# Performance work log

Hardware: AMD Instinct MI355X
Metric: run time of the kernel (lower is better)

## Reference

```python
import jax, jax.numpy as jnp
import numpy as np

MASK_VAL = -1e9

def setup_inputs() -> dict:
    key = jax.random.key(0)
    kq, kk, kv, km = jax.random.split(key, 4)
    bz, lq, lk, d = 16, 2048, 2048, 64
    q = jax.random.normal(kq, (bz, lq, d), dtype=jnp.float32)
    k = jax.random.normal(kk, (bz, lk, d), dtype=jnp.float32)
    v = jax.random.normal(kv, (bz, lk, d), dtype=jnp.float32)
    # pad mask: True = masked-out position
    pad_mask = jax.random.randint(km, (bz, lq, lk), 0, 2) == 1
    return {"q": q, "k": k, "v": v, "pad_mask": pad_mask}

def reference(q, k, v, pad_mask):
    # scores: [bz, lq, lk]
    d = k.shape[-1]
    scores = jnp.einsum('bqd,bkd->bqk', q, k) / jnp.sqrt(jnp.asarray(d, q.dtype))
    scores = jnp.where(pad_mask, jnp.asarray(MASK_VAL, scores.dtype), scores)
    attn = jax.nn.softmax(scores, axis=-1)  # dropout inactive in eval mode
    out = jnp.einsum('bqk,bkd->bqd', attn, v)
    return out
```

## Files before the change

### kernel.cpp

```cpp
#include <hip/hip_runtime.h>
#include <hip/hip_bf16.h>
#include <cstdint>
#include <cstddef>

typedef __attribute__((ext_vector_type(8))) short  short8;
typedef __attribute__((ext_vector_type(4))) short  short4v;
typedef __attribute__((ext_vector_type(4))) float  f32x4;

#define BZ   16
#define LQ   2048
#define LK   2048
#define DD   64
#define QBLK 64
#define KVB  128
#define NIT  (LK / KVB)

__device__ inline short f2bf(float f) {
    union { float f; uint32_t u; } x; x.f = f;
    uint32_t r = x.u + 0x7fffu + ((x.u >> 16) & 1u);
    return (short)(r >> 16);
}

__global__ __launch_bounds__(512, 4)
void attn_fwd(const float* __restrict__ Qg, const float* __restrict__ Kg,
              const float* __restrict__ Vg, const int* __restrict__ Mg,
              float* __restrict__ Og)
{
    __shared__ short Klds[KVB * DD];
    __shared__ short Vtlds[DD * KVB];
    __shared__ short Plds[8][16 * 64];
    __shared__ short Qlds[QBLK * DD];

    const int t = threadIdx.x;
    const int w = t >> 6;
    const int l = t & 63;
    const int g = l >> 4;
    const int n = l & 15;

    const int nb   = blockIdx.x;
    const int xcd  = nb & 7;
    const int jj   = nb >> 3;
    const int b    = xcd + 8 * (jj >> 5);
    const int qtl  = jj & 31;
    const int qbase = qtl * QBLK;

    const int stripe = w & 3;
    const int half   = w >> 2;

    const float* Qb = Qg + ((size_t)b * LQ + qbase) * DD;
    const float* Kb = Kg + (size_t)b * LK * DD;
    const float* Vb = Vg + (size_t)b * LK * DD;
    const int*   Mb = Mg + ((size_t)b * LQ + qbase) * (size_t)LK;

    const int sr = t >> 4;
    const int sc = (t & 15) * 4;

    #pragma unroll
    for (int i = 0; i < 2; ++i) {
        int q = sr + i * 32;
        f32x4 qv = *(const f32x4*)(Qb + (size_t)q * DD + sc);
        short4v qp;
        qp.x = f2bf(qv.x); qp.y = f2bf(qv.y); qp.z = f2bf(qv.z); qp.w = f2bf(qv.w);
        *(short4v*)((char*)Qlds + q * 128 + ((sc * 2) ^ ((q & 7) << 4))) = qp;
    }
    __syncthreads();

    short8 aQ[2];
    {
        int qr = stripe * 16 + n;
        #pragma unroll
        for (int s = 0; s < 2; ++s)
            aQ[s] = *(short8*)((char*)Qlds + qr * 128 + ((s * 64 + g * 16) ^ ((qr & 7) << 4)));
    }

    f32x4 Oacc[4];
    #pragma unroll
    for (int c = 0; c < 4; ++c) { Oacc[c].x = 0.f; Oacc[c].y = 0.f; Oacc[c].z = 0.f; Oacc[c].w = 0.f; }
    float m2[4]   = { -1e30f, -1e30f, -1e30f, -1e30f };
    float lsum[4] = { 0.f, 0.f, 0.f, 0.f };

    const float SC2 = 0.125f * 1.4426950408889634f;

    for (int it = 0; it < NIT; ++it) {
        const int kvbase = it * KVB;

        f32x4 kr[4], vr[4];
        #pragma unroll
        for (int i = 0; i < 4; ++i) {
            int kv = sr + i * 32;
            kr[i] = *(const f32x4*)(Kb + (size_t)(kvbase + kv) * DD + sc);
            vr[i] = *(const f32x4*)(Vb + (size_t)(kvbase + kv) * DD + sc);
        }
        int mv[16];
        #pragma unroll
        for (int r = 0; r < 4; ++r)
            #pragma unroll
            for (int c = 0; c < 4; ++c)
                mv[r * 4 + c] = Mb[(size_t)(stripe * 16 + g * 4 + r) * LK
                                   + kvbase + half * 64 + c * 16 + n];

        __syncthreads();

        #pragma unroll
        for (int i = 0; i < 4; ++i) {
            int kv = sr + i * 32;
            short4v kp;
            kp.x = f2bf(kr[i].x); kp.y = f2bf(kr[i].y); kp.z = f2bf(kr[i].z); kp.w = f2bf(kr[i].w);
            *(short4v*)((char*)Klds + kv * 128 + ((sc * 2) ^ ((kv & 7) << 4))) = kp;
            #pragma unroll
            for (int e = 0; e < 4; ++e) {
                int d = sc + e;
                float fv = (e == 0) ? vr[i].x : (e == 1) ? vr[i].y : (e == 2) ? vr[i].z : vr[i].w;
                *((short*)((char*)Vtlds + d * 256 + ((kv * 2) ^ ((d & 7) << 4)))) = f2bf(fv);
            }
        }
        __syncthreads();

        f32x4 S[4];
        #pragma unroll
        for (int c = 0; c < 4; ++c) { S[c].x = 0.f; S[c].y = 0.f; S[c].z = 0.f; S[c].w = 0.f; }
        #pragma unroll
        for (int c = 0; c < 4; ++c) {
            int kvl = half * 64 + c * 16 + n;
            #pragma unroll
            for (int s = 0; s < 2; ++s) {
                short8 bK = *(short8*)((char*)Klds + kvl * 128
                                       + ((s * 64 + g * 16) ^ ((kvl & 7) << 4)));
                S[c] = __builtin_amdgcn_mfma_f32_16x16x32_bf16(aQ[s], bK, S[c], 0, 0, 0);
            }
        }

        float sv[4][4];
        #pragma unroll
        for (int r = 0; r < 4; ++r)
            #pragma unroll
            for (int c = 0; c < 4; ++c) {
                float x = S[c][r] * SC2;
                sv[r][c] = mv[r * 4 + c] ? -1.0e9f : x;
            }

        #pragma unroll
        for (int r = 0; r < 4; ++r) {
            float mx = fmaxf(fmaxf(sv[r][0], sv[r][1]), fmaxf(sv[r][2], sv[r][3]));
            mx = fmaxf(mx, __shfl_xor(mx, 1));
            mx = fmaxf(mx, __shfl_xor(mx, 2));
            mx = fmaxf(mx, __shfl_xor(mx, 4));
            mx = fmaxf(mx, __shfl_xor(mx, 8));
            float mnew = fmaxf(m2[r], mx);
            float resc = exp2f(m2[r] - mnew);
            m2[r] = mnew;
            lsum[r] *= resc;
            #pragma unroll
            for (int c = 0; c < 4; ++c) Oacc[c][r] *= resc;

            float rs = 0.f;
            int q = g * 4 + r;
            #pragma unroll
            for (int c = 0; c < 4; ++c) {
                float p = exp2f(sv[r][c] - mnew);
                rs += p;
                *((short*)((char*)Plds[w] + q * 128
                           + (((c * 16 + n) * 2) ^ ((q & 7) << 4)))) = f2bf(p);
            }
            rs += __shfl_xor(rs, 1);
            rs += __shfl_xor(rs, 2);
            rs += __shfl_xor(rs, 4);
            rs += __shfl_xor(rs, 8);
            lsum[r] += rs;
        }

        #pragma unroll
        for (int s = 0; s < 2; ++s) {
            short8 aP = *(short8*)((char*)Plds[w] + n * 128
                                   + ((s * 64 + g * 16) ^ ((n & 7) << 4)));
            #pragma unroll
            for (int c = 0; c < 4; ++c) {
                int d = c * 16 + n;
                short8 bV = *(short8*)((char*)Vtlds + d * 256
                                       + ((half * 128 + s * 64 + g * 16) ^ ((d & 7) << 4)));
                Oacc[c] = __builtin_amdgcn_mfma_f32_16x16x32_bf16(aP, bV, Oacc[c], 0, 0, 0);
            }
        }
    }

    __syncthreads();
    float* mrg = (float*)Klds;
    float* mlb = (float*)Vtlds;

    if (half == 1) {
        #pragma unroll
        for (int r = 0; r < 4; ++r) {
            int qloc = g * 4 + r;
            int q = stripe * 16 + qloc;
            if (n == 0) { mlb[q * 2] = m2[r]; mlb[q * 2 + 1] = lsum[r]; }
            #pragma unroll
            for (int c = 0; c < 4; ++c)
                mrg[stripe * 1024 + qloc * 64 + c * 16 + n] = Oacc[c][r];
        }
    }
    __syncthreads();
    if (half == 0) {
        #pragma unroll
        for (int r = 0; r < 4; ++r) {
            int qloc = g * 4 + r;
            int q = stripe * 16 + qloc;
            float mB = mlb[q * 2], lB = mlb[q * 2 + 1];
            float ms = fmaxf(m2[r], mB);
            float sA = exp2f(m2[r] - ms);
            float sB = exp2f(mB - ms);
            float inv = 1.0f / (lsum[r] * sA + lB * sB);
            #pragma unroll
            for (int c = 0; c < 4; ++c) {
                float oB = mrg[stripe * 1024 + qloc * 64 + c * 16 + n];
                Og[((size_t)b * LQ + qbase + q) * DD + c * 16 + n] =
                    (Oacc[c][r] * sA + oB * sB) * inv;
            }
        }
    }
}

extern "C" void kernel_launch(void* const* d_in, const int* in_sizes, int n_in,
                              void* d_out, int out_size, void* d_ws, size_t ws_size,
                              hipStream_t stream) {
    const float* q = (const float*)d_in[0];
    const float* k = (const float*)d_in[1];
    const float* v = (const float*)d_in[2];
    const int*   m = (const int*)d_in[3];
    float* out = (float*)d_out;
    dim3 grid(BZ * (LQ / QBLK) * 1);
    dim3 block(512);
    attn_fwd<<<grid, block, 0, stream>>>(q, k, v, m, out);
}
```

Baseline: 480.0 us.

## Prefetch next K/V and mask tile, vectorize V transpose, use DPP reductions

Global loads of K, V and the mask for the next KV tile are issued right after the LDS barrier, so they overlap with the current tile's MFMA and softmax work instead of stalling at the top of each iteration. V is now loaded column-wise so each thread writes a packed 4-element bf16 vector into the transposed LDS buffer with a 16-row XOR swizzle, replacing scalar short stores. The mask is compressed into a 16-bit register bitfield, and the row max and sum reductions use DPP instead of ds_swizzle shuffles. s_setprio is raised around the MFMA sections. The prefetch increases register pressure under the 512-thread, 4-block launch bound, and the strided scalar V loads may coalesce less well.

```diff
diff --git a/kernel.cpp b/kernel.cpp
--- a/kernel.cpp
+++ b/kernel.cpp
@@ -1,5 +1,4 @@
 #include <hip/hip_runtime.h>
-#include <hip/hip_bf16.h>
 #include <cstdint>
 #include <cstddef>
 
@@ -21,15 +20,34 @@
     return (short)(r >> 16);
 }
 
+template<int CTRL>
+__device__ inline float dppf(float x) {
+    return __int_as_float(__builtin_amdgcn_update_dpp(0, __float_as_int(x), CTRL, 0xF, 0xF, false));
+}
+__device__ inline float rmax16(float x) {
+    x = fmaxf(x, dppf<0xB1>(x));
+    x = fmaxf(x, dppf<0x4E>(x));
+    x = fmaxf(x, dppf<0x124>(x));
+    x = fmaxf(x, dppf<0x128>(x));
+    return x;
+}
+__device__ inline float rsum16(float x) {
+    x += dppf<0xB1>(x);
+    x += dppf<0x4E>(x);
+    x += dppf<0x124>(x);
+    x += dppf<0x128>(x);
+    return x;
+}
+
 __global__ __launch_bounds__(512, 4)
 void attn_fwd(const float* __restrict__ Qg, const float* __restrict__ Kg,
               const float* __restrict__ Vg, const int* __restrict__ Mg,
               float* __restrict__ Og)
 {
-    __shared__ short Klds[KVB * DD];
-    __shared__ short Vtlds[DD * KVB];
-    __shared__ short Plds[8][16 * 64];
-    __shared__ short Qlds[QBLK * DD];
+    __shared__ alignas(128) short Klds[KVB * DD];
+    __shared__ alignas(128) short Vtlds[DD * KVB];
+    __shared__ alignas(128) short Plds[8][16 * 64];
+    __shared__ alignas(128) short Qlds[QBLK * DD];
 
     const int t = threadIdx.x;
     const int w = t >> 6;
@@ -81,24 +99,37 @@
 
     const float SC2 = 0.125f * 1.4426950408889634f;
 
-    for (int it = 0; it < NIT; ++it) {
-        const int kvbase = it * KVB;
-
-        f32x4 kr[4], vr[4];
+    f32x4 kr[4];
+    float vv[4][4];
+    uint32_t mbits;
+
+    auto load_kv = [&](int itx) {
         #pragma unroll
         for (int i = 0; i < 4; ++i) {
             int kv = sr + i * 32;
-            kr[i] = *(const f32x4*)(Kb + (size_t)(kvbase + kv) * DD + sc);
-            vr[i] = *(const f32x4*)(Vb + (size_t)(kvbase + kv) * DD + sc);
-        }
-        int mv[16];
+            kr[i] = *(const f32x4*)(Kb + (size_t)(itx * KVB + kv) * DD + sc);
+        }
+        #pragma unroll
+        for (int p = 0; p < 4; ++p)
+            #pragma unroll
+            for (int e = 0; e < 4; ++e)
+                vv[p][e] = Vb[(size_t)(itx * KVB + p * 32 + w * 4 + e) * DD + l];
+    };
+    auto load_mbits = [&](int itx) -> uint32_t {
+        uint32_t bb = 0;
+        const int* mp = Mb + (size_t)(stripe * 16 + g * 4) * LK + itx * KVB + half * 64 + n;
         #pragma unroll
         for (int r = 0; r < 4; ++r)
             #pragma unroll
             for (int c = 0; c < 4; ++c)
-                mv[r * 4 + c] = Mb[(size_t)(stripe * 16 + g * 4 + r) * LK
-                                   + kvbase + half * 64 + c * 16 + n];
-
+                bb |= (mp[(size_t)r * LK + c * 16] != 0) ? (1u << (r * 4 + c)) : 0u;
+        return bb;
+    };
+
+    load_kv(0);
+    mbits = load_mbits(0);
+
+    for (int it = 0; it < NIT; ++it) {
         __syncthreads();
 
         #pragma unroll
@@ -107,18 +138,25 @@
             short4v kp;
             kp.x = f2bf(kr[i].x); kp.y = f2bf(kr[i].y); kp.z = f2bf(kr[i].z); kp.w = f2bf(kr[i].w);
             *(short4v*)((char*)Klds + kv * 128 + ((sc * 2) ^ ((kv & 7) << 4))) = kp;
-            #pragma unroll
-            for (int e = 0; e < 4; ++e) {
-                int d = sc + e;
-                float fv = (e == 0) ? vr[i].x : (e == 1) ? vr[i].y : (e == 2) ? vr[i].z : vr[i].w;
-                *((short*)((char*)Vtlds + d * 256 + ((kv * 2) ^ ((d & 7) << 4)))) = f2bf(fv);
-            }
+        }
+        #pragma unroll
+        for (int p = 0; p < 4; ++p) {
+            short4v vp;
+            vp.x = f2bf(vv[p][0]); vp.y = f2bf(vv[p][1]);
+            vp.z = f2bf(vv[p][2]); vp.w = f2bf(vv[p][3]);
+            uint32_t byt = (uint32_t)l * 256u
+                         + ((((uint32_t)(p * 32 + w * 4)) * 2u) ^ (((uint32_t)l & 15u) << 4));
+            *(short4v*)((char*)Vtlds + byt) = vp;
         }
         __syncthreads();
 
+        int nx = (it + 1 < NIT) ? it + 1 : it;
+        load_kv(nx);
+
         f32x4 S[4];
         #pragma unroll
         for (int c = 0; c < 4; ++c) { S[c].x = 0.f; S[c].y = 0.f; S[c].z = 0.f; S[c].w = 0.f; }
+        __builtin_amdgcn_s_setprio(1);
         #pragma unroll
         for (int c = 0; c < 4; ++c) {
             int kvl = half * 64 + c * 16 + n;
@@ -129,23 +167,21 @@
                 S[c] = __builtin_amdgcn_mfma_f32_16x16x32_bf16(aQ[s], bK, S[c], 0, 0, 0);
             }
         }
-
-        float sv[4][4];
-        #pragma unroll
-        for (int r = 0; r < 4; ++r)
-            #pragma unroll
-            for (int c = 0; c < 4; ++c) {
+        __builtin_amdgcn_s_setprio(0);
+
+        #pragma unroll
+        for (int c = 0; c < 4; ++c)
+            #pragma unroll
+            for (int r = 0; r < 4; ++r) {
                 float x = S[c][r] * SC2;
-                sv[r][c] = mv[r * 4 + c] ? -1.0e9f : x;
-            }
+                S[c][r] = ((mbits >> (r * 4 + c)) & 1u) ? -1.0e9f : x;
+            }
+        mbits = load_mbits(nx);
 
         #pragma unroll
         for (int r = 0; r < 4; ++r) {
-            float mx = fmaxf(fmaxf(sv[r][0], sv[r][1]), fmaxf(sv[r][2], sv[r][3]));
-            mx = fmaxf(mx, __shfl_xor(mx, 1));
-            mx = fmaxf(mx, __shfl_xor(mx, 2));
-            mx = fmaxf(mx, __shfl_xor(mx, 4));
-            mx = fmaxf(mx, __shfl_xor(mx, 8));
+            float mx = fmaxf(fmaxf(S[0][r], S[1][r]), fmaxf(S[2][r], S[3][r]));
+            mx = rmax16(mx);
             float mnew = fmaxf(m2[r], mx);
             float resc = exp2f(m2[r] - mnew);
             m2[r] = mnew;
@@ -157,18 +193,15 @@
             int q = g * 4 + r;
             #pragma unroll
             for (int c = 0; c < 4; ++c) {
-                float p = exp2f(sv[r][c] - mnew);
+                float p = exp2f(S[c][r] - mnew);
                 rs += p;
                 *((short*)((char*)Plds[w] + q * 128
                            + (((c * 16 + n) * 2) ^ ((q & 7) << 4)))) = f2bf(p);
             }
-            rs += __shfl_xor(rs, 1);
-            rs += __shfl_xor(rs, 2);
-            rs += __shfl_xor(rs, 4);
-            rs += __shfl_xor(rs, 8);
-            lsum[r] += rs;
-        }
-
+            lsum[r] += rsum16(rs);
+        }
+
+        __builtin_amdgcn_s_setprio(1);
         #pragma unroll
         for (int s = 0; s < 2; ++s) {
             short8 aP = *(short8*)((char*)Plds[w] + n * 128
@@ -177,10 +210,11 @@
             for (int c = 0; c < 4; ++c) {
                 int d = c * 16 + n;
                 short8 bV = *(short8*)((char*)Vtlds + d * 256
-                                       + ((half * 128 + s * 64 + g * 16) ^ ((d & 7) << 4)));
+                                       + (((half * 128 + s * 64 + g * 16)) ^ ((d & 15) << 4)));
                 Oacc[c] = __builtin_amdgcn_mfma_f32_16x16x32_bf16(aP, bV, Oacc[c], 0, 0, 0);
             }
         }
+        __builtin_amdgcn_s_setprio(0);
     }
 
     __syncthreads();
@@ -227,7 +261,7 @@
     const float* v = (const float*)d_in[2];
     const int*   m = (const int*)d_in[3];
     float* out = (float*)d_out;
-    dim3 grid(BZ * (LQ / QBLK) * 1);
+    dim3 grid(BZ * (LQ / QBLK));
     dim3 block(512);
     attn_fwd<<<grid, block, 0, stream>>>(q, k, v, m, out);
 }
```

Result: slower. 535.2 us (+11.5%).
